# Performance work log

Measured on AMD Instinct MI355X. Metric: run time of the kernel, lower is better.

## Reference

```python
import jax, jax.numpy as jnp
import numpy as np

L, N, E, H = 4096, 1, 1024, 16
DH = E // H
SCALE = DH ** -0.5


def setup_inputs() -> dict:
    key = jax.random.key(0)
    k1, k2, k3 = jax.random.split(key, 3)
    # xavier_uniform-ish scales for faithfulness of magnitude
    lim_qkv = (6.0 / (3 * E + E)) ** 0.5
    lim_out = (6.0 / (E + E)) ** 0.5
    x = jax.random.normal(k1, (L, N, E), dtype=jnp.float32)
    w_qkv = jax.random.uniform(k2, (3 * E, E), dtype=jnp.float32, minval=-lim_qkv, maxval=lim_qkv)
    w_out = jax.random.uniform(k3, (E, E), dtype=jnp.float32, minval=-lim_out, maxval=lim_out)
    return {"x": x, "w_qkv": w_qkv, "w_out": w_out}


def reference(x, w_qkv, w_out):
    # x: [L, N, E]
    qkv = jnp.einsum('lne,fe->lnf', x, w_qkv)          # [L, N, 3E]
    q, k, v = jnp.split(qkv, 3, axis=-1)               # each [L, N, E]

    def to_heads(t):
        # [L, N, E] -> [N*H, L, DH]
        return t.reshape(L, N * H, DH).transpose(1, 0, 2)

    q = to_heads(q) * SCALE
    k = to_heads(k)
    v = to_heads(v)
    attn = jnp.einsum('bld,bmd->blm', q, k)            # [N*H, L, L]
    attn = jax.nn.softmax(attn, axis=-1)
    out = jnp.einsum('blm,bmd->bld', attn, v)          # [N*H, L, DH]
    out = out.transpose(1, 0, 2).reshape(L, N, E)
    return jnp.einsum('lne,fe->lnf', out, w_out)       # [L, N, E]
```

## Files before the change

kernel.cpp:

```cpp
#include <hip/hip_runtime.h>
#include <hip/hip_bf16.h>
#include <stdint.h>

#define L_SEQ 4096
#define EMB   1024
#define NHEAD 16
#define DHEAD 64

#define SM_SCALE 0.18033688011112042f
#define SM_FIXED_MAX 12.0f

typedef __attribute__((ext_vector_type(8))) short short8;
typedef __attribute__((ext_vector_type(4))) short s16x4;
typedef __attribute__((ext_vector_type(4))) float f32x4;
typedef __attribute__((ext_vector_type(2))) unsigned uint2v;

struct Pack8 { f32x4 lo, hi; };

__device__ inline short f2bf(float f) {
  union { float f; unsigned u; } c; c.f = f;
  unsigned r = (c.u + 0x7fffu + ((c.u >> 16) & 1u)) >> 16;
  return (short)(unsigned short)r;
}
__device__ inline unsigned fbits(float f) {
  union { float f; unsigned u; } c; c.f = f; return c.u;
}
__device__ inline unsigned pack_trunc(float f0, float f1) {
#if __has_builtin(__builtin_amdgcn_perm)
  return __builtin_amdgcn_perm(fbits(f1), fbits(f0), 0x07060302u);
#else
  return (fbits(f0) >> 16) | (fbits(f1) & 0xffff0000u);
#endif
}

#if __has_builtin(__builtin_amdgcn_exp2f)
#define EXP2F(x) __builtin_amdgcn_exp2f(x)
#else
#define EXP2F(x) exp2f(x)
#endif

template<bool F32>
__device__ inline auto ld8(const void* p, size_t off) {
  if constexpr (F32) {
    const float* f = (const float*)p + off;
    Pack8 r; r.lo = *(const f32x4*)f; r.hi = *(const f32x4*)(f + 4);
    return r;
  } else {
    return *(const short8*)((const short*)p + off);
  }
}
__device__ inline short8 cvt8(Pack8 r) {
  short8 o;
#pragma unroll
  for (int j = 0; j < 4; ++j) { o[j] = f2bf(r.lo[j]); o[4 + j] = f2bf(r.hi[j]); }
  return o;
}
__device__ inline short8 cvt8(short8 r) { return r; }

#define MFMA16(a, b, c) __builtin_amdgcn_mfma_f32_16x16x32_bf16(a, b, c, 0, 0, 0)
#define FZERO ((f32x4){0.f, 0.f, 0.f, 0.f})

__global__ __launch_bounds__(256)
void conv_kernel(const float* __restrict__ in, short* __restrict__ out, int n) {
  int i = (blockIdx.x * 256 + threadIdx.x) * 8;
  if (i >= n) return;
  Pack8 r; r.lo = *(const f32x4*)(in + i); r.hi = *(const f32x4*)(in + i + 4);
  *(short8*)(out + i) = cvt8(r);
}

template<bool AF32, bool BF32, bool CF32>
__global__ __launch_bounds__(256, 2)
void gemm_bt(const void* __restrict__ Av, const void* __restrict__ Bv,
             void* __restrict__ Cv, int N, int K, int lda, int ldc,
             float cscale) {
  __shared__ __align__(16) short At[128 * 40];
  __shared__ __align__(16) short Bt[128 * 40];

  const int tid  = threadIdx.x;
  const int lane = tid & 63;
  const int wave = tid >> 6;
  const int quad = lane >> 4;
  const int l15  = lane & 15;
  const int q8   = quad << 3;

  const int nbn = N >> 7;
  const int bm  = (blockIdx.x / nbn) << 7;
  const int bn  = (blockIdx.x % nbn) << 7;
  const int wr  = wave >> 1;
  const int wc  = wave & 1;

  const int s0 = tid, s1 = tid + 256;
  const int ar0 = s0 >> 2, ac0 = (s0 & 3) << 3;
  const int ar1 = s1 >> 2, ac1 = (s1 & 3) << 3;

  const size_t aoff0 = (size_t)(bm + ar0) * lda + ac0;
  const size_t aoff1 = (size_t)(bm + ar1) * lda + ac1;
  const size_t boff0 = (size_t)(bn + ar0) * K + ac0;
  const size_t boff1 = (size_t)(bn + ar1) * K + ac1;

  f32x4 acc[4][4];
#pragma unroll
  for (int r = 0; r < 4; ++r)
#pragma unroll
    for (int c = 0; c < 4; ++c) acc[r][c] = FZERO;

  auto ga0 = ld8<AF32>(Av, aoff0);
  auto ga1 = ld8<AF32>(Av, aoff1);
  auto gb0 = ld8<BF32>(Bv, boff0);
  auto gb1 = ld8<BF32>(Bv, boff1);

  const int arow = (wr * 64 + l15) * 40 + q8;
  const int brow = (wc * 64 + l15) * 40 + q8;

  const int nk = K >> 5;
  for (int kt = 0; kt < nk; ++kt) {
    __syncthreads();
    *(short8*)(At + ar0 * 40 + ac0) = cvt8(ga0);
    *(short8*)(At + ar1 * 40 + ac1) = cvt8(ga1);
    *(short8*)(Bt + ar0 * 40 + ac0) = cvt8(gb0);
    *(short8*)(Bt + ar1 * 40 + ac1) = cvt8(gb1);
    __syncthreads();

    if (kt + 1 < nk) {
      const size_t k0 = (size_t)(kt + 1) << 5;
      ga0 = ld8<AF32>(Av, aoff0 + k0);
      ga1 = ld8<AF32>(Av, aoff1 + k0);
      gb0 = ld8<BF32>(Bv, boff0 + k0);
      gb1 = ld8<BF32>(Bv, boff1 + k0);
    }

    short8 af[4], bf[4];
#pragma unroll
    for (int r = 0; r < 4; ++r) af[r] = *(const short8*)(At + arow + r * 640);
#pragma unroll
    for (int c = 0; c < 4; ++c) bf[c] = *(const short8*)(Bt + brow + c * 640);
#pragma unroll
    for (int r = 0; r < 4; ++r)
#pragma unroll
      for (int c = 0; c < 4; ++c)
        acc[r][c] = MFMA16(af[r], bf[c], acc[r][c]);
  }

#pragma unroll
  for (int r = 0; r < 4; ++r) {
#pragma unroll
    for (int c = 0; c < 4; ++c) {
      const int col = bn + wc * 64 + c * 16 + l15;
#pragma unroll
      for (int reg = 0; reg < 4; ++reg) {
        const int row = bm + wr * 64 + r * 16 + quad * 4 + reg;
        const float v = acc[r][c][reg] * cscale;
        if constexpr (CF32) ((float*)Cv)[(size_t)row * ldc + col] = v;
        else                ((short*)Cv)[(size_t)row * ldc + col] = f2bf(v);
      }
    }
  }
}

__global__ __launch_bounds__(256, 2)
void gemm_qkv(const short* __restrict__ A, const float* __restrict__ B,
              short* __restrict__ qb, short* __restrict__ kb,
              short* __restrict__ vt) {
  __shared__ __align__(16) short At[128 * 40];
  __shared__ __align__(16) short Bt[128 * 40];

  const int tid  = threadIdx.x;
  const int lane = tid & 63;
  const int wave = tid >> 6;
  const int quad = lane >> 4;
  const int l15  = lane & 15;
  const int q8   = quad << 3;

  const int bm  = (blockIdx.x / 24) << 7;
  const int bn  = (blockIdx.x % 24) << 7;
  const int wr  = wave >> 1;
  const int wc  = wave & 1;

  const int s0 = tid, s1 = tid + 256;
  const int ar0 = s0 >> 2, ac0 = (s0 & 3) << 3;
  const int ar1 = s1 >> 2, ac1 = (s1 & 3) << 3;

  const size_t aoff0 = (size_t)(bm + ar0) * EMB + ac0;
  const size_t aoff1 = (size_t)(bm + ar1) * EMB + ac1;
  const size_t boff0 = (size_t)(bn + ar0) * EMB + ac0;
  const size_t boff1 = (size_t)(bn + ar1) * EMB + ac1;

  f32x4 acc[4][4];
#pragma unroll
  for (int r = 0; r < 4; ++r)
#pragma unroll
    for (int c = 0; c < 4; ++c) acc[r][c] = FZERO;

  short8 ga0 = *(const short8*)(A + aoff0);
  short8 ga1 = *(const short8*)(A + aoff1);
  Pack8  gb0 = ld8<true>(B, boff0);
  Pack8  gb1 = ld8<true>(B, boff1);

  const int arow = (wr * 64 + l15) * 40 + q8;
  const int brow = (wc * 64 + l15) * 40 + q8;

  for (int kt = 0; kt < 32; ++kt) {
    __syncthreads();
    *(short8*)(At + ar0 * 40 + ac0) = ga0;
    *(short8*)(At + ar1 * 40 + ac1) = ga1;
    *(short8*)(Bt + ar0 * 40 + ac0) = cvt8(gb0);
    *(short8*)(Bt + ar1 * 40 + ac1) = cvt8(gb1);
    __syncthreads();

    if (kt + 1 < 32) {
      const size_t k0 = (size_t)(kt + 1) << 5;
      ga0 = *(const short8*)(A + aoff0 + k0);
      ga1 = *(const short8*)(A + aoff1 + k0);
      gb0 = ld8<true>(B, boff0 + k0);
      gb1 = ld8<true>(B, boff1 + k0);
    }

    short8 af[4], bf[4];
#pragma unroll
    for (int r = 0; r < 4; ++r) af[r] = *(const short8*)(At + arow + r * 640);
#pragma unroll
    for (int c = 0; c < 4; ++c) bf[c] = *(const short8*)(Bt + brow + c * 640);
#pragma unroll
    for (int r = 0; r < 4; ++r)
#pragma unroll
      for (int c = 0; c < 4; ++c)
        acc[r][c] = MFMA16(af[r], bf[c], acc[r][c]);
  }

  if (bn < 2048) {
    short* dst = (bn < 1024) ? qb : kb;
    const int bcol = (bn < 1024) ? bn : bn - 1024;
    const float cs = (bn < 1024) ? SM_SCALE : 1.0f;
#pragma unroll
    for (int r = 0; r < 4; ++r)
#pragma unroll
      for (int c = 0; c < 4; ++c) {
        const int col = bcol + wc * 64 + c * 16 + l15;
#pragma unroll
        for (int reg = 0; reg < 4; ++reg) {
          const int row = bm + wr * 64 + r * 16 + quad * 4 + reg;
          dst[(size_t)row * EMB + col] = f2bf(acc[r][c][reg] * cs);
        }
      }
  } else {
    const int bcol = bn - 2048;
#pragma unroll
    for (int r = 0; r < 4; ++r)
#pragma unroll
      for (int c = 0; c < 4; ++c) {
        const int col  = bcol + wc * 64 + c * 16 + l15;
        const int rowb = bm + wr * 64 + r * 16 + quad * 4;
        s16x4 pk;
#pragma unroll
        for (int reg = 0; reg < 4; ++reg) pk[reg] = f2bf(acc[r][c][reg]);
        *(s16x4*)(vt + (size_t)col * L_SEQ + rowb) = pk;
      }
  }
}

__global__ __launch_bounds__(256, 2)
void attn_kernel(short* __restrict__ qo, const short* __restrict__ kbuf,
                 const short* __restrict__ vtbuf) {
  __shared__ __align__(16) short Kt[2][64 * 72];
  __shared__ __align__(16) short Vt[2][64 * 72];
  __shared__ __align__(16) short PQ[128 * 72];

  const int tid  = threadIdx.x;
  const int lane = tid & 63;
  const int w    = tid >> 6;
  const int quad = lane >> 4;
  const int l15  = lane & 15;
  const int q8   = quad << 3;

  const int h    = blockIdx.x >> 5;
  const int qblk = blockIdx.x & 31;
  const int hcol = h * 64;

  const int srow = tid >> 3;
  const int sc8  = (tid & 7) << 3;

#pragma unroll
  for (int rr = 0; rr < 4; ++rr) {
    const int row = srow + rr * 32;
    short8 g = *(const short8*)(qo + (size_t)(qblk * 128 + row) * EMB + hcol + sc8);
    *(short8*)(PQ + row * 72 + sc8) = g;
  }
  __syncthreads();

  short8 qf[2][2];
#pragma unroll
  for (int g = 0; g < 2; ++g) {
    const int qrow = (w * 32 + g * 16 + l15) * 72;
    qf[g][0] = *(const short8*)(PQ + qrow + q8);
    qf[g][1] = *(const short8*)(PQ + qrow + 32 + q8);
  }

  const short8 vone = {0x3F80, 0x3F80, 0x3F80, 0x3F80,
                       0x3F80, 0x3F80, 0x3F80, 0x3F80};

  f32x4 o[2][4];
#pragma unroll
  for (int g = 0; g < 2; ++g)
#pragma unroll
    for (int f = 0; f < 4; ++f) o[g][f] = FZERO;
  f32x4 l_c[2] = {FZERO, FZERO};

  short* const pw = PQ + w * (32 * 72);
  const int prow = l15 * 72;

  const size_t koff0 = (size_t)srow * EMB + hcol + sc8;
  const size_t voff0 = (size_t)(hcol + srow) * L_SEQ + sc8;
  const size_t krr = (size_t)32 * EMB;
  const size_t vrr = (size_t)32 * L_SEQ;

  short8 gk0 = *(const short8*)(kbuf + koff0);
  short8 gk1 = *(const short8*)(kbuf + koff0 + krr);
  short8 gv0 = *(const short8*)(vtbuf + voff0);
  short8 gv1 = *(const short8*)(vtbuf + voff0 + vrr);

  for (int t = 0; t < 64; ++t) {
    short* const ktb = &Kt[t & 1][0];
    short* const vtb = &Vt[t & 1][0];

    *(short8*)(ktb + srow * 72 + sc8) = gk0;
    *(short8*)(ktb + (srow + 32) * 72 + sc8) = gk1;
    *(short8*)(vtb + srow * 72 + sc8) = gv0;
    *(short8*)(vtb + (srow + 32) * 72 + sc8) = gv1;
    __syncthreads();

    if (t < 63) {
      const size_t kk = (size_t)(t + 1) * 64;
      gk0 = *(const short8*)(kbuf + koff0 + kk * EMB);
      gk1 = *(const short8*)(kbuf + koff0 + krr + kk * EMB);
      gv0 = *(const short8*)(vtbuf + voff0 + kk);
      gv1 = *(const short8*)(vtbuf + voff0 + vrr + kk);
    }

    f32x4 s[2][4];
#pragma unroll
    for (int f = 0; f < 4; ++f) {
      const int krow = (f * 16 + l15) * 72;
      short8 kf0 = *(const short8*)(ktb + krow + q8);
      short8 kf1 = *(const short8*)(ktb + krow + 32 + q8);
      s[0][f] = MFMA16(kf0, qf[0][0], FZERO);
      s[0][f] = MFMA16(kf1, qf[0][1], s[0][f]);
      s[1][f] = MFMA16(kf0, qf[1][0], FZERO);
      s[1][f] = MFMA16(kf1, qf[1][1], s[1][f]);
    }

    short8 pa[2][2];
#pragma unroll
    for (int g = 0; g < 2; ++g) {
      float p[4][4];
#pragma unroll
      for (int f = 0; f < 4; ++f)
#pragma unroll
        for (int r = 0; r < 4; ++r)
          p[f][r] = EXP2F(s[g][f][r] - SM_FIXED_MAX);

      short* const pg = pw + g * (16 * 72);
#pragma unroll
      for (int f = 0; f < 4; ++f) {
        uint2v pk = { pack_trunc(p[f][0], p[f][1]), pack_trunc(p[f][2], p[f][3]) };
        *(uint2v*)(pg + prow + f * 16 + quad * 4) = pk;
      }
      pa[g][0] = *(const short8*)(pg + prow + q8);
      pa[g][1] = *(const short8*)(pg + prow + 32 + q8);

      f32x4 rsv = MFMA16(pa[g][0], vone, FZERO);
      rsv = MFMA16(pa[g][1], vone, rsv);
#pragma unroll
      for (int r = 0; r < 4; ++r) l_c[g][r] += rsv[r];
    }

#pragma unroll
    for (int f = 0; f < 4; ++f) {
      const int vrow = (f * 16 + l15) * 72;
      short8 v0 = *(const short8*)(vtb + vrow + q8);
      short8 v1 = *(const short8*)(vtb + vrow + 32 + q8);
      o[0][f] = MFMA16(pa[0][0], v0, o[0][f]);
      o[0][f] = MFMA16(pa[0][1], v1, o[0][f]);
      o[1][f] = MFMA16(pa[1][0], v0, o[1][f]);
      o[1][f] = MFMA16(pa[1][1], v1, o[1][f]);
    }
  }

#pragma unroll
  for (int g = 0; g < 2; ++g) {
    f32x4 inv;
#pragma unroll
    for (int r = 0; r < 4; ++r) inv[r] = 1.0f / l_c[g][r];
    short* const pg = pw + g * (16 * 72);
#pragma unroll
    for (int f = 0; f < 4; ++f)
#pragma unroll
      for (int r = 0; r < 4; ++r)
        pg[(quad * 4 + r) * 72 + f * 16 + l15] = f2bf(o[g][f][r] * inv[r]);
  }

#pragma unroll
  for (int rr = 0; rr < 4; ++rr) {
    const int row = (lane >> 3) + rr * 8;
    const int c8  = (lane & 7) << 3;
    short8 g = *(const short8*)(pw + row * 72 + c8);
    *(short8*)(qo + (size_t)(qblk * 128 + w * 32 + row) * EMB + hcol + c8) = g;
  }
}

extern "C" void kernel_launch(void* const* d_in, const int* in_sizes, int n_in,
                              void* d_out, int out_size, void* d_ws, size_t ws_size,
                              hipStream_t stream) {
  (void)in_sizes; (void)n_in; (void)out_size; (void)ws_size;
  const float* x     = (const float*)d_in[0];
  const float* w_qkv = (const float*)d_in[1];
  const float* w_out = (const float*)d_in[2];

  short* qbuf  = (short*)d_ws;
  short* x_bf  = qbuf + (size_t)L_SEQ * EMB;
  short* wo_bf = x_bf;
  short* kbuf  = (short*)d_out;
  short* vtbuf = kbuf + (size_t)L_SEQ * EMB;
  float* outp  = (float*)d_out;

  conv_kernel<<<dim3(L_SEQ * EMB / 2048), 256, 0, stream>>>(x, x_bf, L_SEQ * EMB);

  gemm_qkv<<<dim3(768), 256, 0, stream>>>(x_bf, w_qkv, qbuf, kbuf, vtbuf);

  conv_kernel<<<dim3(EMB * EMB / 2048), 256, 0, stream>>>(w_out, wo_bf, EMB * EMB);

  attn_kernel<<<dim3(NHEAD * (L_SEQ / 128)), 256, 0, stream>>>(qbuf, kbuf, vtbuf);

  gemm_bt<false, false, true><<<dim3(256), 256, 0, stream>>>(qbuf, wo_bf, outp, EMB, EMB, EMB, EMB, 1.0f);
}
```

Measured before the change: 229.4 us.

## Replace LDS round-trip of P with permlane16 swaps and load Q directly

The softmax probabilities are no longer written to shared memory and read back in MFMA A-operand layout. Instead, register-level v_permlane16_swap exchanges rearrange the packed bf16 values, and the V fragment column indexing is permuted to match the new k-ordering. Q fragments are loaded straight from global memory, and the output staging buffer now reuses Kt after a barrier, so the PQ shared array is dropped. This removes LDS traffic and latency from the inner loop and cuts shared memory use, which could allow more occupancy. The cost is a dependence on gfx950 permlane instructions and correctness that rests on matching the permuted k-order between P and V.

Result: faster. 220.2 us (-4.0%).

```diff
diff --git a/kernel.cpp b/kernel.cpp
--- a/kernel.cpp
+++ b/kernel.cpp
@@ -38,6 +38,21 @@
 #else
 #define EXP2F(x) exp2f(x)
 #endif
+
+__device__ inline void pl16swap(unsigned &x, unsigned &y) {
+#if __has_builtin(__builtin_amdgcn_permlane16_swap)
+  auto r = __builtin_amdgcn_permlane16_swap(x, y, false, false);
+  x = r[0]; y = r[1];
+#else
+  asm volatile("v_permlane16_swap_b32 %0, %1" : "+v"(x), "+v"(y));
+#endif
+}
+
+__device__ inline short8 mk8(unsigned d0, unsigned d1, unsigned d2, unsigned d3) {
+  union { unsigned u[4]; short8 s; } c;
+  c.u[0] = d0; c.u[1] = d1; c.u[2] = d2; c.u[3] = d3;
+  return c.s;
+}
 
 template<bool F32>
 __device__ inline auto ld8(const void* p, size_t off) {
@@ -263,7 +278,6 @@
                  const short* __restrict__ vtbuf) {
   __shared__ __align__(16) short Kt[2][64 * 72];
   __shared__ __align__(16) short Vt[2][64 * 72];
-  __shared__ __align__(16) short PQ[128 * 72];
 
   const int tid  = threadIdx.x;
   const int lane = tid & 63;
@@ -271,6 +285,7 @@
   const int quad = lane >> 4;
   const int l15  = lane & 15;
   const int q8   = quad << 3;
+  const int vb   = ((quad & 1) << 4) | ((quad >> 1) << 3);
 
   const int h    = blockIdx.x >> 5;
   const int qblk = blockIdx.x & 31;
@@ -279,20 +294,12 @@
   const int srow = tid >> 3;
   const int sc8  = (tid & 7) << 3;
 
-#pragma unroll
-  for (int rr = 0; rr < 4; ++rr) {
-    const int row = srow + rr * 32;
-    short8 g = *(const short8*)(qo + (size_t)(qblk * 128 + row) * EMB + hcol + sc8);
-    *(short8*)(PQ + row * 72 + sc8) = g;
-  }
-  __syncthreads();
-
   short8 qf[2][2];
 #pragma unroll
   for (int g = 0; g < 2; ++g) {
-    const int qrow = (w * 32 + g * 16 + l15) * 72;
-    qf[g][0] = *(const short8*)(PQ + qrow + q8);
-    qf[g][1] = *(const short8*)(PQ + qrow + 32 + q8);
+    const short* qp = qo + (size_t)(qblk * 128 + w * 32 + g * 16 + l15) * EMB + hcol;
+    qf[g][0] = *(const short8*)(qp + q8);
+    qf[g][1] = *(const short8*)(qp + 32 + q8);
   }
 
   const short8 vone = {0x3F80, 0x3F80, 0x3F80, 0x3F80,
@@ -304,9 +311,6 @@
 #pragma unroll
     for (int f = 0; f < 4; ++f) o[g][f] = FZERO;
   f32x4 l_c[2] = {FZERO, FZERO};
-
-  short* const pw = PQ + w * (32 * 72);
-  const int prow = l15 * 72;
 
   const size_t koff0 = (size_t)srow * EMB + hcol + sc8;
   const size_t voff0 = (size_t)(hcol + srow) * L_SEQ + sc8;
@@ -358,14 +362,18 @@
         for (int r = 0; r < 4; ++r)
           p[f][r] = EXP2F(s[g][f][r] - SM_FIXED_MAX);
 
-      short* const pg = pw + g * (16 * 72);
+      unsigned pk[4][2];
 #pragma unroll
       for (int f = 0; f < 4; ++f) {
-        uint2v pk = { pack_trunc(p[f][0], p[f][1]), pack_trunc(p[f][2], p[f][3]) };
-        *(uint2v*)(pg + prow + f * 16 + quad * 4) = pk;
+        pk[f][0] = pack_trunc(p[f][0], p[f][1]);
+        pk[f][1] = pack_trunc(p[f][2], p[f][3]);
       }
-      pa[g][0] = *(const short8*)(pg + prow + q8);
-      pa[g][1] = *(const short8*)(pg + prow + 32 + q8);
+      pl16swap(pk[0][0], pk[1][0]);
+      pl16swap(pk[0][1], pk[1][1]);
+      pl16swap(pk[2][0], pk[3][0]);
+      pl16swap(pk[2][1], pk[3][1]);
+      pa[g][0] = mk8(pk[0][0], pk[0][1], pk[1][0], pk[1][1]);
+      pa[g][1] = mk8(pk[2][0], pk[2][1], pk[3][0], pk[3][1]);
 
       f32x4 rsv = MFMA16(pa[g][0], vone, FZERO);
       rsv = MFMA16(pa[g][1], vone, rsv);
@@ -376,8 +384,8 @@
 #pragma unroll
     for (int f = 0; f < 4; ++f) {
       const int vrow = (f * 16 + l15) * 72;
-      short8 v0 = *(const short8*)(vtb + vrow + q8);
-      short8 v1 = *(const short8*)(vtb + vrow + 32 + q8);
+      short8 v0 = *(const short8*)(vtb + vrow + vb);
+      short8 v1 = *(const short8*)(vtb + vrow + 32 + vb);
       o[0][f] = MFMA16(pa[0][0], v0, o[0][f]);
       o[0][f] = MFMA16(pa[0][1], v1, o[0][f]);
       o[1][f] = MFMA16(pa[1][0], v0, o[1][f]);
@@ -385,6 +393,8 @@
     }
   }
 
+  __syncthreads();
+  short* const pw = &Kt[0][0] + w * (32 * 72);
 #pragma unroll
   for (int g = 0; g < 2; ++g) {
     f32x4 inv;
@@ -402,8 +412,8 @@
   for (int rr = 0; rr < 4; ++rr) {
     const int row = (lane >> 3) + rr * 8;
     const int c8  = (lane & 7) << 3;
-    short8 g = *(const short8*)(pw + row * 72 + c8);
-    *(short8*)(qo + (size_t)(qblk * 128 + w * 32 + row) * EMB + hcol + c8) = g;
+    short8 gv = *(const short8*)(pw + row * 72 + c8);
+    *(short8*)(qo + (size_t)(qblk * 128 + w * 32 + row) * EMB + hcol + c8) = gv;
   }
 }
 
```
